# Optimization experiments

Measured on AMD Instinct MI355X. Metric: run time of the kernel, lower is better.

Reference implementation:

```python
import jax, jax.numpy as jnp
import numpy as np

DIM = 1024
HEADS = 16
SEQ = 1024
N_EXP = 2
SLOTS = SEQ // N_EXP  # slots per expert; total slots == seq_len as in SoftMoE(dim, seq_len, num_experts)
HID = 4 * DIM         # expert FFN hidden
EPS = 1e-5


def layernorm(x, g, b):
    mu = x.mean(-1, keepdims=True)
    var = x.var(-1, keepdims=True)
    return (x - mu) * jax.lax.rsqrt(var + EPS) * g + b


def setup_inputs() -> dict:
    key = jax.random.key(0)
    ks = jax.random.split(key, 16)
    s = lambda k, shape, scale=0.02: jax.random.normal(k, shape, jnp.float32) * scale
    return {
        "x": jax.random.normal(ks[0], (4, SEQ, DIM), jnp.float32),
        "Wq": s(ks[1], (DIM, DIM)), "bq": jnp.zeros((DIM,), jnp.float32),
        "Wkv": s(ks[2], (DIM, 2 * DIM)), "bkv": jnp.zeros((2 * DIM,), jnp.float32),
        "Wp": s(ks[3], (DIM, DIM)), "bp": jnp.zeros((DIM,), jnp.float32),
        "g1": jnp.ones((DIM,), jnp.float32), "b1": jnp.zeros((DIM,), jnp.float32),
        "phi": s(ks[4], (DIM, N_EXP, SLOTS)),
        "We1": s(ks[5], (N_EXP, DIM, HID)), "be1": jnp.zeros((N_EXP, HID), jnp.float32),
        "We2": s(ks[6], (N_EXP, HID, DIM)), "be2": jnp.zeros((N_EXP, DIM), jnp.float32),
        "g2": jnp.ones((DIM,), jnp.float32), "b2": jnp.zeros((DIM,), jnp.float32),
    }


def soft_moe(x, phi, We1, be1, We2, be2):
    # x: [b,n,d]; phi: [d,e,s]
    logits = jnp.einsum("bnd,des->bnes", x, phi)
    dispatch = jax.nn.softmax(logits, axis=1)                    # over sequence
    b, n, e, s = logits.shape
    combine = jax.nn.softmax(logits.reshape(b, n, e * s), axis=-1).reshape(b, n, e, s)
    slots = jnp.einsum("bnd,bnes->besd", x, dispatch)            # [b,e,s,d]
    h = jax.nn.gelu(jnp.einsum("besd,edh->besh", slots, We1) + be1[None, :, None, :])
    y = jnp.einsum("besh,ehd->besd", h, We2) + be2[None, :, None, :]
    return jnp.einsum("besd,bnes->bnd", y, combine)


def reference(x, Wq, bq, Wkv, bkv, Wp, bp, g1, b1, phi, We1, be1, We2, be2, g2, b2):
    b, n, c = x.shape
    hd = c // HEADS
    scale = hd ** -0.5
    q = (x @ Wq + bq).reshape(b, n, HEADS, hd)
    kv = (x @ Wkv + bkv).reshape(b, n, 2, HEADS, hd)
    k, v = kv[:, :, 0], kv[:, :, 1]
    attn = jnp.einsum("bnhd,bmhd->bnmh", q, k) * scale
    attn = jax.nn.softmax(attn, axis=2)
    out = jnp.einsum("bnmh,bmhd->bnhd", attn, v).reshape(b, n, c)
    out = out @ Wp + bp
    x1 = layernorm(out + x, g1, b1)
    x2 = x1 + soft_moe(x1, phi, We1, be1, We2, be2)
    y = layernorm(x2 + x1, g2, b2)
    return (y, attn)
```

## Files before the change

### kernel.cpp

```cpp
#include <hip/hip_runtime.h>
#include <math.h>

#define BATCH 4
#define SEQ   1024
#define DIM   1024
#define HEADS 16
#define HD    64
#define NEXP  2
#define NSLOT 512
#define ES    1024
#define HID   4096
#define LNEPS 1e-5f
#define NTOK  (BATCH*SEQ)

typedef long long ll;
typedef unsigned short ushort;
typedef unsigned int uint;
typedef __attribute__((ext_vector_type(8))) short short8;
typedef __attribute__((ext_vector_type(4))) float f32x4;
typedef __attribute__((ext_vector_type(4))) unsigned short us4;

__device__ __forceinline__ ushort f2b(float f) {
    uint u = __builtin_bit_cast(uint, f);
    u += 0x7FFFu + ((u >> 16) & 1u);
    return (ushort)(u >> 16);
}
__device__ __forceinline__ float b2f(ushort h) {
    uint u = ((uint)h) << 16;
    return __builtin_bit_cast(float, u);
}
__device__ __forceinline__ uint pk(float a, float b) {
    return (uint)f2b(a) | ((uint)f2b(b) << 16);
}
__device__ __forceinline__ float gelu_f(float v) {
    float x3 = v * v * v;
    return 0.5f * v * (1.f + tanhf(0.7978845608028654f * (v + 0.044715f * x3)));
}

__device__ __forceinline__ void gload16(const ushort* g, ushort* l) {
    __builtin_amdgcn_global_load_lds(
        (const __attribute__((address_space(1))) unsigned int*)(const void*)g,
        (__attribute__((address_space(3))) unsigned int*)(void*)l,
        16, 0, 0);
}

__global__ __launch_bounds__(256) void cvt_bf16(
    const float* __restrict__ src, ushort* __restrict__ dst)
{
    int i = blockIdx.x * 256 + threadIdx.x;
    const float4* s = reinterpret_cast<const float4*>(src) + (ll)i * 2;
    float4 a = s[0], b = s[1];
    uint4 w;
    w.x = pk(a.x, a.y); w.y = pk(a.z, a.w);
    w.z = pk(b.x, b.y); w.w = pk(b.z, b.w);
    reinterpret_cast<uint4*>(dst)[i] = w;
}

__global__ __launch_bounds__(256) void concat_bias(
    const float* __restrict__ a, const float* __restrict__ b,
    float* __restrict__ o)
{
    int i = blockIdx.x * 256 + threadIdx.x;
    o[i] = (i < DIM) ? a[i] : b[i - DIM];
}

template<typename TS>
__global__ __launch_bounds__(256) void transpose_cvt(
    const TS* __restrict__ src, int ldsrc, ll sS1, ll sS2,
    ushort* __restrict__ dst, int lddst, ll sD1, ll sD2, int Z2)
{
    __shared__ ushort tile[64][68];
    const int z1 = blockIdx.z / Z2, z2 = blockIdx.z % Z2;
    src += z1 * sS1 + z2 * sS2;
    dst += z1 * sD1 + z2 * sD2;
    const int r0 = blockIdx.y * 64, c0 = blockIdx.x * 64;
    const int t = threadIdx.x;
    #pragma unroll
    for (int j = 0; j < 4; j++) {
        int idx = t + 256 * j;
        int r = idx >> 4, c = (idx & 15) * 4;
        if constexpr (sizeof(TS) == 4) {
            float4 v = *reinterpret_cast<const float4*>(src + (ll)(r0 + r) * ldsrc + c0 + c);
            tile[r][c]     = f2b(v.x);
            tile[r][c + 1] = f2b(v.y);
            tile[r][c + 2] = f2b(v.z);
            tile[r][c + 3] = f2b(v.w);
        } else {
            *reinterpret_cast<us4*>(&tile[r][c]) =
                *reinterpret_cast<const us4*>(src + (ll)(r0 + r) * ldsrc + c0 + c);
        }
    }
    __syncthreads();
    #pragma unroll
    for (int j = 0; j < 4; j++) {
        int idx = t + 256 * j;
        int rr = idx >> 4, cc = (idx & 15) * 4;
        us4 w;
        w.x = tile[cc][rr]; w.y = tile[cc + 1][rr];
        w.z = tile[cc + 2][rr]; w.w = tile[cc + 3][rr];
        *reinterpret_cast<us4*>(&dst[(ll)(c0 + rr) * lddst + r0 + cc]) = w;
    }
}

template<int WR, int WC, int MI, int NI, int ACT, typename TC>
__global__ __launch_bounds__(256) void gemm_bf16(
    const ushort* __restrict__ A, int lda, ll sA1, ll sA2,
    const ushort* __restrict__ B, int ldb, ll sB1, ll sB2,
    const float* __restrict__ bias, ll sb1, ll sb2,
    TC* __restrict__ C, int ldc, ll sC1, ll sC2,
    int K, int Z2, float alpha)
{
    constexpr int BM = WR * MI * 16;
    constexpr int BN = WC * NI * 16;
    __shared__ alignas(16) ushort As[BM * 32];
    __shared__ alignas(16) ushort Bs[BN * 32];

    const int z1 = blockIdx.z / Z2, z2 = blockIdx.z % Z2;
    A += z1 * sA1 + z2 * sA2;
    B += z1 * sB1 + z2 * sB2;
    C += z1 * sC1 + z2 * sC2;

    const int t = threadIdx.x;
    const int m0 = blockIdx.y * BM, n0 = blockIdx.x * BN;
    const int lane = t & 63, wave = t >> 6;
    const int quad = lane >> 4, l16 = lane & 15;
    const int wm = wave / WC, wn = wave % WC;

    f32x4 acc[MI][NI] = {};

    for (int k0 = 0; k0 < K; k0 += 32) {
        #pragma unroll
        for (int i = 0; i < BM / 64; i++) {
            int seg = i * 256 + t;
            int row = seg >> 2, ke = (seg & 3) * 8;
            gload16(A + (ll)(m0 + row) * lda + (k0 + ke), &As[seg * 8]);
        }
        #pragma unroll
        for (int i = 0; i < BN / 64; i++) {
            int seg = i * 256 + t;
            int row = seg >> 2, ke = (seg & 3) * 8;
            gload16(B + (ll)(n0 + row) * ldb + (k0 + ke), &Bs[seg * 8]);
        }
        __syncthreads();

        short8 a[MI], b[NI];
        #pragma unroll
        for (int mi = 0; mi < MI; mi++)
            a[mi] = *reinterpret_cast<const short8*>(
                &As[(wm * MI * 16 + mi * 16 + l16) * 32 + quad * 8]);
        #pragma unroll
        for (int ni = 0; ni < NI; ni++)
            b[ni] = *reinterpret_cast<const short8*>(
                &Bs[(wn * NI * 16 + ni * 16 + l16) * 32 + quad * 8]);
        #pragma unroll
        for (int mi = 0; mi < MI; mi++)
            #pragma unroll
            for (int ni = 0; ni < NI; ni++)
                acc[mi][ni] = __builtin_amdgcn_mfma_f32_16x16x32_bf16(
                    a[mi], b[ni], acc[mi][ni], 0, 0, 0);
        __syncthreads();
    }

    const float* bz = bias ? (bias + z1 * sb1 + z2 * sb2) : nullptr;
    #pragma unroll
    for (int mi = 0; mi < MI; mi++) {
        #pragma unroll
        for (int ni = 0; ni < NI; ni++) {
            const int row = m0 + wm * MI * 16 + mi * 16 + quad * 4;
            const int col = n0 + wn * NI * 16 + ni * 16 + l16;
            const float bv = bz ? bz[col] : 0.f;
            #pragma unroll
            for (int r = 0; r < 4; r++) {
                float v = alpha * acc[mi][ni][r] + bv;
                if (ACT) v = gelu_f(v);
                if constexpr (sizeof(TC) == 2)
                    C[(ll)(row + r) * ldc + col] = f2b(v);
                else
                    C[(ll)(row + r) * ldc + col] = v;
            }
        }
    }
}

template<int BM, int BN, int ACT, typename TC>
__global__ __launch_bounds__(512) void gemm2(
    const ushort* __restrict__ A, int lda, ll sA1, ll sA2,
    const ushort* __restrict__ B, int ldb, ll sB1, ll sB2,
    const float* __restrict__ bias, ll sb1, ll sb2,
    TC* __restrict__ C, int ldc, ll sC1, ll sC2,
    int K, int Z2, float alpha)
{
    constexpr int WR = BM / 64;
    constexpr int WC = 8 / WR;
    constexpr int MI = 4;
    constexpr int NI = BN / WC / 16;
    constexpr int NH = NI / 2 ? NI / 2 : 1;
    constexpr int LA = BM / 64;
    constexpr int LB = BN / 64;

    __shared__ alignas(16) ushort As[3][BM * 64];
    __shared__ alignas(16) ushort Bs[3][BN * 64];

    const int z1 = blockIdx.z / Z2, z2 = blockIdx.z % Z2;
    A += z1 * sA1 + z2 * sA2;
    B += z1 * sB1 + z2 * sB2;
    C += z1 * sC1 + z2 * sC2;

    const int t = threadIdx.x;
    const int lane = t & 63, wave = t >> 6;
    const int quad = lane >> 4, l16 = lane & 15;
    const int wm = wave / WC, wn = wave % WC;
    const int m0 = blockIdx.y * BM, n0 = blockIdx.x * BN;

    auto stageA = [&](int kt) {
        const ushort* src = A + (ll)m0 * lda + kt * 64;
        ushort* dst = As[kt % 3];
        #pragma unroll
        for (int j = 0; j < LA; j++) {
            int seg = j * 512 + t;
            int row = seg >> 3, kk = (seg & 7) * 8;
            gload16(src + (ll)row * lda + kk, dst + seg * 8);
        }
    };
    auto stageB = [&](int kt) {
        const ushort* src = B + (ll)n0 * ldb + kt * 64;
        ushort* dst = Bs[kt % 3];
        #pragma unroll
        for (int j = 0; j < LB; j++) {
            int seg = j * 512 + t;
            int row = seg >> 3, kk = (seg & 7) * 8;
            gload16(src + (ll)row * ldb + kk, dst + seg * 8);
        }
    };

    f32x4 acc[MI][NI] = {};
    const int NK = K / 64;

    stageA(0); stageB(0);
    if (NK > 1) { stageA(1); stageB(1); }

    for (int kt = 0; kt < NK; kt++) {
        if (kt + 1 < NK)
            asm volatile("s_waitcnt vmcnt(%0)" :: "n"(LA + LB) : "memory");
        else
            asm volatile("s_waitcnt vmcnt(0)" ::: "memory");
        __builtin_amdgcn_sched_barrier(0);
        __builtin_amdgcn_s_barrier();
        __builtin_amdgcn_sched_barrier(0);

        const ushort* Abuf = As[kt % 3];
        const ushort* Bbuf = Bs[kt % 3];

        short8 a[MI][2], b0[NH][2];
        #pragma unroll
        for (int mi = 0; mi < MI; mi++)
            #pragma unroll
            for (int kh = 0; kh < 2; kh++)
                a[mi][kh] = *reinterpret_cast<const short8*>(
                    &Abuf[(wm * 64 + mi * 16 + l16) * 64 + kh * 32 + quad * 8]);
        #pragma unroll
        for (int ni = 0; ni < NH; ni++)
            #pragma unroll
            for (int kh = 0; kh < 2; kh++)
                b0[ni][kh] = *reinterpret_cast<const short8*>(
                    &Bbuf[(wn * NI * 16 + ni * 16 + l16) * 64 + kh * 32 + quad * 8]);
        if (kt + 2 < NK) stageA(kt + 2);
        asm volatile("s_waitcnt lgkmcnt(0)" ::: "memory");
        __builtin_amdgcn_sched_barrier(0);
        __builtin_amdgcn_s_setprio(1);
        #pragma unroll
        for (int mi = 0; mi < MI; mi++)
            #pragma unroll
            for (int ni = 0; ni < NH; ni++)
                #pragma unroll
                for (int kh = 0; kh < 2; kh++)
                    acc[mi][ni] = __builtin_amdgcn_mfma_f32_16x16x32_bf16(
                        a[mi][kh], b0[ni][kh], acc[mi][ni], 0, 0, 0);
        __builtin_amdgcn_s_setprio(0);
        __builtin_amdgcn_sched_barrier(0);

        short8 b1[NH][2];
        #pragma unroll
        for (int ni = 0; ni < NH; ni++)
            #pragma unroll
            for (int kh = 0; kh < 2; kh++)
                b1[ni][kh] = *reinterpret_cast<const short8*>(
                    &Bbuf[(wn * NI * 16 + (NH + ni) * 16 + l16) * 64 + kh * 32 + quad * 8]);
        if (kt + 2 < NK) stageB(kt + 2);
        asm volatile("s_waitcnt lgkmcnt(0)" ::: "memory");
        __builtin_amdgcn_sched_barrier(0);
        __builtin_amdgcn_s_setprio(1);
        #pragma unroll
        for (int mi = 0; mi < MI; mi++)
            #pragma unroll
            for (int ni = 0; ni < NH; ni++)
                #pragma unroll
                for (int kh = 0; kh < 2; kh++)
                    acc[mi][NH + ni] = __builtin_amdgcn_mfma_f32_16x16x32_bf16(
                        a[mi][kh], b1[ni][kh], acc[mi][NH + ni], 0, 0, 0);
        __builtin_amdgcn_s_setprio(0);
        __builtin_amdgcn_sched_barrier(0);
    }

    const float* bz = bias ? (bias + z1 * sb1 + z2 * sb2) : nullptr;
    #pragma unroll
    for (int mi = 0; mi < MI; mi++) {
        #pragma unroll
        for (int ni = 0; ni < NI; ni++) {
            const int row = m0 + wm * 64 + mi * 16 + quad * 4;
            const int col = n0 + wn * NI * 16 + ni * 16 + l16;
            const float bv = bz ? bz[col] : 0.f;
            #pragma unroll
            for (int r = 0; r < 4; r++) {
                float v = alpha * acc[mi][ni][r] + bv;
                if (ACT) v = gelu_f(v);
                if constexpr (sizeof(TC) == 2)
                    C[(ll)(row + r) * ldc + col] = f2b(v);
                else
                    C[(ll)(row + r) * ldc + col] = v;
            }
        }
    }
}

__global__ __launch_bounds__(256) void attn_softmax(
    ushort* __restrict__ p, float* __restrict__ attn_out)
{
    __shared__ float tile[16][1024];
    const int n = blockIdx.x, b = blockIdx.y;
    const int t = threadIdx.x;
    const int lane = t & 63, w = t >> 6;
    ushort* base = p + ((ll)(b * SEQ + n) * HEADS) * SEQ;
    #pragma unroll 1
    for (int g = 0; g < 4; g++) {
        const int h = g * 4 + w;
        ushort* row = base + (ll)h * SEQ + lane * 16;
        uint4 r0 = reinterpret_cast<const uint4*>(row)[0];
        uint4 r1 = reinterpret_cast<const uint4*>(row)[1];
        uint rr[8] = {r0.x, r0.y, r0.z, r0.w, r1.x, r1.y, r1.z, r1.w};
        float v[16];
        float m = -3.0e38f;
        #pragma unroll
        for (int j = 0; j < 8; j++) {
            v[2 * j]     = b2f((ushort)(rr[j] & 0xFFFFu));
            v[2 * j + 1] = b2f((ushort)(rr[j] >> 16));
            m = fmaxf(m, fmaxf(v[2 * j], v[2 * j + 1]));
        }
        #pragma unroll
        for (int o = 32; o; o >>= 1) m = fmaxf(m, __shfl_xor(m, o));
        float s = 0.f;
        #pragma unroll
        for (int j = 0; j < 16; j++) { v[j] = __expf(v[j] - m); s += v[j]; }
        #pragma unroll
        for (int o = 32; o; o >>= 1) s += __shfl_xor(s, o);
        const float inv = 1.f / s;
        #pragma unroll
        for (int j = 0; j < 16; j++) v[j] *= inv;
        uint pw[8];
        #pragma unroll
        for (int j = 0; j < 8; j++) pw[j] = pk(v[2 * j], v[2 * j + 1]);
        uint4 w0, w1;
        w0.x = pw[0]; w0.y = pw[1]; w0.z = pw[2]; w0.w = pw[3];
        w1.x = pw[4]; w1.y = pw[5]; w1.z = pw[6]; w1.w = pw[7];
        reinterpret_cast<uint4*>(row)[0] = w0;
        reinterpret_cast<uint4*>(row)[1] = w1;
        #pragma unroll
        for (int jj = 0; jj < 4; jj++) {
            float4 f4;
            f4.x = v[4 * jj]; f4.y = v[4 * jj + 1];
            f4.z = v[4 * jj + 2]; f4.w = v[4 * jj + 3];
            *reinterpret_cast<float4*>(&tile[h][(jj * 64 + lane) * 4]) = f4;
        }
    }
    __syncthreads();
    float* outp = attn_out + ((ll)b * SEQ + n) * SEQ * HEADS;
    #pragma unroll
    for (int jj = 0; jj < 4; jj++) {
        const int mm = t + 256 * jj;
        const int gm = mm >> 2;
        const int fi = ((gm & 3) * 64 + (gm >> 2)) * 4 + (mm & 3);
        float o16[16];
        #pragma unroll
        for (int h = 0; h < 16; h++) o16[h] = tile[h][fi];
        float4* dst = reinterpret_cast<float4*>(outp + (ll)mm * HEADS);
        #pragma unroll
        for (int q = 0; q < 4; q++) {
            float4 o4;
            o4.x = o16[4 * q]; o4.y = o16[4 * q + 1];
            o4.z = o16[4 * q + 2]; o4.w = o16[4 * q + 3];
            dst[q] = o4;
        }
    }
}

__global__ __launch_bounds__(256) void ln_kernel(
    const float* __restrict__ a, const float* __restrict__ b, float coef,
    const float* __restrict__ g, const float* __restrict__ beta,
    float* __restrict__ out, ushort* __restrict__ out_bf)
{
    const int row = blockIdx.x;
    const int t = threadIdx.x;
    float4 av = reinterpret_cast<const float4*>(a + (ll)row * DIM)[t];
    float4 bv = reinterpret_cast<const float4*>(b + (ll)row * DIM)[t];
    float4 v;
    v.x = av.x + coef * bv.x; v.y = av.y + coef * bv.y;
    v.z = av.z + coef * bv.z; v.w = av.w + coef * bv.w;
    float s1 = v.x + v.y + v.z + v.w;
    float s2 = v.x * v.x + v.y * v.y + v.z * v.z + v.w * v.w;
    __shared__ float red[8];
    #pragma unroll
    for (int o = 32; o; o >>= 1) { s1 += __shfl_xor(s1, o); s2 += __shfl_xor(s2, o); }
    int w = t >> 6;
    if ((t & 63) == 0) { red[w] = s1; red[4 + w] = s2; }
    __syncthreads();
    s1 = red[0] + red[1] + red[2] + red[3];
    s2 = red[4] + red[5] + red[6] + red[7];
    float mu = s1 * (1.f / DIM);
    float var = s2 * (1.f / DIM) - mu * mu;
    float rs = rsqrtf(var + LNEPS);
    float4 gv = reinterpret_cast<const float4*>(g)[t];
    float4 be = reinterpret_cast<const float4*>(beta)[t];
    float4 o;
    o.x = (v.x - mu) * rs * gv.x + be.x;
    o.y = (v.y - mu) * rs * gv.y + be.y;
    o.z = (v.z - mu) * rs * gv.z + be.z;
    o.w = (v.w - mu) * rs * gv.w + be.w;
    reinterpret_cast<float4*>(out + (ll)row * DIM)[t] = o;
    if (out_bf) {
        us4 hv;
        hv.x = f2b(o.x); hv.y = f2b(o.y); hv.z = f2b(o.z); hv.w = f2b(o.w);
        reinterpret_cast<us4*>(out_bf + (ll)row * DIM)[t] = hv;
    }
}

__global__ __launch_bounds__(256) void col_softmax(
    const float* __restrict__ logits, ushort* __restrict__ dispT)
{
    const int b = blockIdx.x, cc = blockIdx.y;
    const int cl = threadIdx.x & 63;
    const int c = cc * 64 + cl;
    const int rg = threadIdx.x >> 6;
    const float* L = logits + (ll)b * SEQ * ES + c;
    ushort* DT = dispT + (ll)b * ES * SEQ + (ll)c * SEQ;
    __shared__ float red[4][64];
    float m = -3.0e38f;
    for (int n = rg; n < SEQ; n += 4) m = fmaxf(m, L[(ll)n * ES]);
    red[rg][cl] = m;
    __syncthreads();
    m = fmaxf(fmaxf(red[0][cl], red[1][cl]), fmaxf(red[2][cl], red[3][cl]));
    __syncthreads();
    float s = 0.f;
    for (int n = rg; n < SEQ; n += 4) s += __expf(L[(ll)n * ES] - m);
    red[rg][cl] = s;
    __syncthreads();
    s = red[0][cl] + red[1][cl] + red[2][cl] + red[3][cl];
    float inv = 1.f / s;
    for (int n = rg; n < SEQ; n += 4)
        DT[n] = f2b(__expf(L[(ll)n * ES] - m) * inv);
}

__global__ __launch_bounds__(256) void row_softmax(
    const float* __restrict__ logits, ushort* __restrict__ comb)
{
    const int row = blockIdx.x;
    const float* L = logits + (ll)row * ES;
    ushort* O = comb + (ll)row * ES;
    float v[4];
    float m = -3.0e38f;
    #pragma unroll
    for (int j = 0; j < 4; j++) { v[j] = L[threadIdx.x + 256 * j]; m = fmaxf(m, v[j]); }
    __shared__ float red[8];
    #pragma unroll
    for (int o = 32; o; o >>= 1) m = fmaxf(m, __shfl_xor(m, o));
    int w = threadIdx.x >> 6;
    if ((threadIdx.x & 63) == 0) red[w] = m;
    __syncthreads();
    m = fmaxf(fmaxf(red[0], red[1]), fmaxf(red[2], red[3]));
    __syncthreads();
    float s = 0.f;
    #pragma unroll
    for (int j = 0; j < 4; j++) { v[j] = __expf(v[j] - m); s += v[j]; }
    #pragma unroll
    for (int o = 32; o; o >>= 1) s += __shfl_xor(s, o);
    if ((threadIdx.x & 63) == 0) red[4 + w] = s;
    __syncthreads();
    s = red[4] + red[5] + red[6] + red[7];
    float inv = 1.f / s;
    #pragma unroll
    for (int j = 0; j < 4; j++) O[threadIdx.x + 256 * j] = f2b(v[j] * inv);
}

extern "C" void kernel_launch(void* const* d_in, const int* in_sizes, int n_in,
                              void* d_out, int out_size, void* d_ws, size_t ws_size,
                              hipStream_t stream)
{
    const float* x   = (const float*)d_in[0];
    const float* Wq  = (const float*)d_in[1];
    const float* bq  = (const float*)d_in[2];
    const float* Wkv = (const float*)d_in[3];
    const float* bkv = (const float*)d_in[4];
    const float* Wp  = (const float*)d_in[5];
    const float* bp  = (const float*)d_in[6];
    const float* g1  = (const float*)d_in[7];
    const float* b1  = (const float*)d_in[8];
    const float* phi = (const float*)d_in[9];
    const float* We1 = (const float*)d_in[10];
    const float* be1 = (const float*)d_in[11];
    const float* We2 = (const float*)d_in[12];
    const float* be2 = (const float*)d_in[13];
    const float* g2  = (const float*)d_in[14];
    const float* b2  = (const float*)d_in[15];

    float* out_y    = (float*)d_out;
    float* out_attn = out_y + (ll)BATCH * SEQ * DIM;

    const ll M1 = 1024 * 1024;
    float*  ws     = (float*)d_ws;
    ushort* x_bf   = (ushort*)(ws);
    ushort* WqkvT  = (ushort*)(ws + 2 * M1);
    ushort* WpT    = (ushort*)(ws + 7 * M1 / 2);
    ushort* phiT   = (ushort*)(ws + 4 * M1);
    ushort* qkv_bf = (ushort*)(ws + 9 * M1 / 2);
    ushort* vT     = (ushort*)(ws + 21 * M1 / 2);
    ushort* p_bf   = (ushort*)(ws + 25 * M1 / 2);
    float*  po     = ws + 25 * M1 / 2;
    ushort* ao_bf  = (ushort*)(ws + 89 * M1 / 2);
    ushort* ymoeT  = (ushort*)(ws + 89 * M1 / 2);
    float*  x1     = ws + 33 * M1 / 2;
    ushort* x1_bf  = (ushort*)(ws + 41 * M1 / 2);
    ushort* x1T    = (ushort*)(ws + 45 * M1 / 2);
    float*  logit  = ws + 49 * M1 / 2;
    ushort* dispT  = (ushort*)(ws + 57 * M1 / 2);
    ushort* comb   = (ushort*)(ws + 61 * M1 / 2);
    ushort* slots  = (ushort*)(ws + 65 * M1 / 2);
    ushort* hmid   = (ushort*)(ws + 69 * M1 / 2);
    ushort* ymoe   = (ushort*)(ws + 85 * M1 / 2);
    ushort* We1T   = (ushort*)(ws + 9 * M1 / 2);
    ushort* We2T   = (ushort*)(ws + 17 * M1 / 2);
    float*  bqkv   = ws + 93 * M1 / 2;
    float*  moe    = ws;

    dim3 blk(256), blk5(512);

    cvt_bf16<<<dim3(2048), blk, 0, stream>>>(x, x_bf);
    transpose_cvt<float><<<dim3(16, 16, 1), blk, 0, stream>>>(
        Wq, DIM, 0, 0, WqkvT, DIM, 0, 0, 1);
    transpose_cvt<float><<<dim3(32, 16, 1), blk, 0, stream>>>(
        Wkv, 2 * DIM, 0, 0, WqkvT + (ll)DIM * DIM, DIM, 0, 0, 1);
    transpose_cvt<float><<<dim3(16, 16, 1), blk, 0, stream>>>(
        Wp, DIM, 0, 0, WpT, DIM, 0, 0, 1);
    transpose_cvt<float><<<dim3(16, 16, 1), blk, 0, stream>>>(
        phi, ES, 0, 0, phiT, DIM, 0, 0, 1);
    concat_bias<<<dim3(12), blk, 0, stream>>>(bq, bkv, bqkv);

    gemm2<256,128,0,ushort><<<dim3(24, 16, 1), blk5, 0, stream>>>(
        x_bf, DIM, 0, 0, WqkvT, DIM, 0, 0, bqkv, 0, 0,
        qkv_bf, 3 * DIM, 0, 0, DIM, 1, 1.f);

    transpose_cvt<ushort><<<dim3(1, 16, BATCH * HEADS), blk, 0, stream>>>(
        qkv_bf + 2 * DIM, 3 * DIM, (ll)SEQ * 3 * DIM, HD,
        vT, SEQ, (ll)HEADS * HD * SEQ, (ll)HD * SEQ, HEADS);

    gemm_bf16<2,2,4,4,0,ushort><<<dim3(8, 8, BATCH * HEADS), blk, 0, stream>>>(
        qkv_bf, 3 * DIM, (ll)SEQ * 3 * DIM, HD,
        qkv_bf + DIM, 3 * DIM, (ll)SEQ * 3 * DIM, HD,
        nullptr, 0, 0,
        p_bf, HEADS * SEQ, (ll)SEQ * HEADS * SEQ, (ll)SEQ,
        HD, HEADS, 0.125f);

    attn_softmax<<<dim3(SEQ, BATCH), blk, 0, stream>>>(p_bf, out_attn);

    gemm_bf16<4,1,2,4,0,ushort><<<dim3(1, 8, BATCH * HEADS), blk, 0, stream>>>(
        p_bf, HEADS * SEQ, (ll)SEQ * HEADS * SEQ, (ll)SEQ,
        vT, SEQ, (ll)HEADS * HD * SEQ, (ll)HD * SEQ,
        nullptr, 0, 0,
        ao_bf, DIM, (ll)SEQ * DIM, HD,
        SEQ, HEADS, 1.f);

    gemm2<128,128,0,float><<<dim3(8, 32, 1), blk5, 0, stream>>>(
        ao_bf, DIM, 0, 0, WpT, DIM, 0, 0, bp, 0, 0,
        po, DIM, 0, 0, DIM, 1, 1.f);
    ln_kernel<<<dim3(NTOK), blk, 0, stream>>>(po, x, 1.0f, g1, b1, x1, x1_bf);

    transpose_cvt<float><<<dim3(64, 16, 2), blk, 0, stream>>>(
        We1, HID, 0, (ll)DIM * HID, We1T, DIM, 0, (ll)HID * DIM, 2);
    transpose_cvt<float><<<dim3(16, 64, 2), blk, 0, stream>>>(
        We2, DIM, 0, (ll)HID * DIM, We2T, HID, 0, (ll)DIM * HID, 2);
    transpose_cvt<ushort><<<dim3(16, 16, BATCH), blk, 0, stream>>>(
        x1_bf, DIM, (ll)SEQ * DIM, 0, x1T, SEQ, (ll)DIM * SEQ, 0, 1);

    gemm2<128,128,0,float><<<dim3(8, 32, 1), blk5, 0, stream>>>(
        x1_bf, DIM, 0, 0, phiT, DIM, 0, 0, nullptr, 0, 0,
        logit, ES, 0, 0, DIM, 1, 1.f);
    col_softmax<<<dim3(BATCH, 16), blk, 0, stream>>>(logit, dispT);
    row_softmax<<<dim3(NTOK), blk, 0, stream>>>(logit, comb);

    gemm2<128,128,0,ushort><<<dim3(8, 8, BATCH), blk5, 0, stream>>>(
        dispT, SEQ, (ll)ES * SEQ, 0,
        x1T, SEQ, (ll)DIM * SEQ, 0,
        nullptr, 0, 0,
        slots, DIM, (ll)ES * DIM, 0,
        SEQ, 1, 1.f);

    gemm2<256,128,1,ushort><<<dim3(32, 2, BATCH * NEXP), blk5, 0, stream>>>(
        slots, DIM, (ll)ES * DIM, (ll)NSLOT * DIM,
        We1T, DIM, 0, (ll)HID * DIM,
        be1, 0, HID,
        hmid, HID, (ll)ES * HID, (ll)NSLOT * HID,
        DIM, NEXP, 1.f);

    gemm2<128,128,0,ushort><<<dim3(8, 4, BATCH * NEXP), blk5, 0, stream>>>(
        hmid, HID, (ll)ES * HID, (ll)NSLOT * HID,
        We2T, HID, 0, (ll)DIM * HID,
        be2, 0, DIM,
        ymoe, DIM, (ll)ES * DIM, (ll)NSLOT * DIM,
        HID, NEXP, 1.f);

    transpose_cvt<ushort><<<dim3(16, 16, BATCH), blk, 0, stream>>>(
        ymoe, DIM, (ll)ES * DIM, 0, ymoeT, ES, (ll)DIM * ES, 0, 1);

    gemm2<128,128,0,float><<<dim3(8, 8, BATCH), blk5, 0, stream>>>(
        comb, ES, (ll)SEQ * ES, 0,
        ymoeT, ES, (ll)DIM * ES, 0,
        nullptr, 0, 0,
        moe, DIM, (ll)SEQ * DIM, 0,
        ES, 1, 1.f);

    ln_kernel<<<dim3(NTOK), blk, 0, stream>>>(moe, x1, 2.0f, g2, b2, out_y, nullptr);
}
```

Baseline: 1.003 ms.

## Replace column softmax with fp32 transpose plus row softmax; use gemm2 for PV

The column-wise dispatch softmax ran in only 64 blocks with strided loads. It is replaced by an fp32 tiled transpose of the logits into a reused workspace region, followed by the vectorised row softmax kernel over BATCH*ES rows. The transpose kernel is generalised to support a float destination, and row_softmax now uses float4 loads and us4 stores. The attention P·V GEMM also moves from gemm_bf16 to the larger-tile gemm2 kernel. This costs an extra transpose pass over the logits and relies on the po/p_bf workspace region being free at that point.

```diff
diff --git a/kernel.cpp b/kernel.cpp
--- a/kernel.cpp
+++ b/kernel.cpp
@@ -64,12 +64,12 @@
     o[i] = (i < DIM) ? a[i] : b[i - DIM];
 }
 
-template<typename TS>
+template<typename TS, typename TD>
 __global__ __launch_bounds__(256) void transpose_cvt(
     const TS* __restrict__ src, int ldsrc, ll sS1, ll sS2,
-    ushort* __restrict__ dst, int lddst, ll sD1, ll sD2, int Z2)
-{
-    __shared__ ushort tile[64][68];
+    TD* __restrict__ dst, int lddst, ll sD1, ll sD2, int Z2)
+{
+    __shared__ TD tile[64][68];
     const int z1 = blockIdx.z / Z2, z2 = blockIdx.z % Z2;
     src += z1 * sS1 + z2 * sS2;
     dst += z1 * sD1 + z2 * sD2;
@@ -79,12 +79,15 @@
     for (int j = 0; j < 4; j++) {
         int idx = t + 256 * j;
         int r = idx >> 4, c = (idx & 15) * 4;
-        if constexpr (sizeof(TS) == 4) {
+        if constexpr (sizeof(TS) == 4 && sizeof(TD) == 2) {
             float4 v = *reinterpret_cast<const float4*>(src + (ll)(r0 + r) * ldsrc + c0 + c);
             tile[r][c]     = f2b(v.x);
             tile[r][c + 1] = f2b(v.y);
             tile[r][c + 2] = f2b(v.z);
             tile[r][c + 3] = f2b(v.w);
+        } else if constexpr (sizeof(TS) == 4 && sizeof(TD) == 4) {
+            float4 v = *reinterpret_cast<const float4*>(src + (ll)(r0 + r) * ldsrc + c0 + c);
+            *reinterpret_cast<float4*>(&tile[r][c]) = v;
         } else {
             *reinterpret_cast<us4*>(&tile[r][c]) =
                 *reinterpret_cast<const us4*>(src + (ll)(r0 + r) * ldsrc + c0 + c);
@@ -95,10 +98,17 @@
     for (int j = 0; j < 4; j++) {
         int idx = t + 256 * j;
         int rr = idx >> 4, cc = (idx & 15) * 4;
-        us4 w;
-        w.x = tile[cc][rr]; w.y = tile[cc + 1][rr];
-        w.z = tile[cc + 2][rr]; w.w = tile[cc + 3][rr];
-        *reinterpret_cast<us4*>(&dst[(ll)(c0 + rr) * lddst + r0 + cc]) = w;
+        if constexpr (sizeof(TD) == 2) {
+            us4 w;
+            w.x = tile[cc][rr]; w.y = tile[cc + 1][rr];
+            w.z = tile[cc + 2][rr]; w.w = tile[cc + 3][rr];
+            *reinterpret_cast<us4*>(&dst[(ll)(c0 + rr) * lddst + r0 + cc]) = w;
+        } else {
+            float4 w;
+            w.x = tile[cc][rr]; w.y = tile[cc + 1][rr];
+            w.z = tile[cc + 2][rr]; w.w = tile[cc + 3][rr];
+            *reinterpret_cast<float4*>(&dst[(ll)(c0 + rr) * lddst + r0 + cc]) = w;
+        }
     }
 }
 
@@ -433,61 +443,35 @@
     }
 }
 
-__global__ __launch_bounds__(256) void col_softmax(
-    const float* __restrict__ logits, ushort* __restrict__ dispT)
-{
-    const int b = blockIdx.x, cc = blockIdx.y;
-    const int cl = threadIdx.x & 63;
-    const int c = cc * 64 + cl;
-    const int rg = threadIdx.x >> 6;
-    const float* L = logits + (ll)b * SEQ * ES + c;
-    ushort* DT = dispT + (ll)b * ES * SEQ + (ll)c * SEQ;
-    __shared__ float red[4][64];
-    float m = -3.0e38f;
-    for (int n = rg; n < SEQ; n += 4) m = fmaxf(m, L[(ll)n * ES]);
-    red[rg][cl] = m;
-    __syncthreads();
-    m = fmaxf(fmaxf(red[0][cl], red[1][cl]), fmaxf(red[2][cl], red[3][cl]));
-    __syncthreads();
-    float s = 0.f;
-    for (int n = rg; n < SEQ; n += 4) s += __expf(L[(ll)n * ES] - m);
-    red[rg][cl] = s;
-    __syncthreads();
-    s = red[0][cl] + red[1][cl] + red[2][cl] + red[3][cl];
-    float inv = 1.f / s;
-    for (int n = rg; n < SEQ; n += 4)
-        DT[n] = f2b(__expf(L[(ll)n * ES] - m) * inv);
-}
-
 __global__ __launch_bounds__(256) void row_softmax(
     const float* __restrict__ logits, ushort* __restrict__ comb)
 {
     const int row = blockIdx.x;
-    const float* L = logits + (ll)row * ES;
-    ushort* O = comb + (ll)row * ES;
-    float v[4];
-    float m = -3.0e38f;
-    #pragma unroll
-    for (int j = 0; j < 4; j++) { v[j] = L[threadIdx.x + 256 * j]; m = fmaxf(m, v[j]); }
+    const int t = threadIdx.x;
+    float4 v = reinterpret_cast<const float4*>(logits + (ll)row * 1024)[t];
+    float m = fmaxf(fmaxf(v.x, v.y), fmaxf(v.z, v.w));
     __shared__ float red[8];
     #pragma unroll
     for (int o = 32; o; o >>= 1) m = fmaxf(m, __shfl_xor(m, o));
-    int w = threadIdx.x >> 6;
-    if ((threadIdx.x & 63) == 0) red[w] = m;
+    int w = t >> 6;
+    if ((t & 63) == 0) red[w] = m;
     __syncthreads();
     m = fmaxf(fmaxf(red[0], red[1]), fmaxf(red[2], red[3]));
     __syncthreads();
-    float s = 0.f;
-    #pragma unroll
-    for (int j = 0; j < 4; j++) { v[j] = __expf(v[j] - m); s += v[j]; }
+    float4 e;
+    e.x = __expf(v.x - m); e.y = __expf(v.y - m);
+    e.z = __expf(v.z - m); e.w = __expf(v.w - m);
+    float s = e.x + e.y + e.z + e.w;
     #pragma unroll
     for (int o = 32; o; o >>= 1) s += __shfl_xor(s, o);
-    if ((threadIdx.x & 63) == 0) red[4 + w] = s;
+    if ((t & 63) == 0) red[4 + w] = s;
     __syncthreads();
     s = red[4] + red[5] + red[6] + red[7];
     float inv = 1.f / s;
-    #pragma unroll
-    for (int j = 0; j < 4; j++) O[threadIdx.x + 256 * j] = f2b(v[j] * inv);
+    us4 hv;
+    hv.x = f2b(e.x * inv); hv.y = f2b(e.y * inv);
+    hv.z = f2b(e.z * inv); hv.w = f2b(e.w * inv);
+    reinterpret_cast<us4*>(comb + (ll)row * 1024)[t] = hv;
 }
 
 extern "C" void kernel_launch(void* const* d_in, const int* in_sizes, int n_in,
@@ -524,6 +508,7 @@
     ushort* vT     = (ushort*)(ws + 21 * M1 / 2);
     ushort* p_bf   = (ushort*)(ws + 25 * M1 / 2);
     float*  po     = ws + 25 * M1 / 2;
+    float*  logitT = ws + 25 * M1 / 2;
     ushort* ao_bf  = (ushort*)(ws + 89 * M1 / 2);
     ushort* ymoeT  = (ushort*)(ws + 89 * M1 / 2);
     float*  x1     = ws + 33 * M1 / 2;
@@ -543,13 +528,13 @@
     dim3 blk(256), blk5(512);
 
     cvt_bf16<<<dim3(2048), blk, 0, stream>>>(x, x_bf);
-    transpose_cvt<float><<<dim3(16, 16, 1), blk, 0, stream>>>(
+    transpose_cvt<float,ushort><<<dim3(16, 16, 1), blk, 0, stream>>>(
         Wq, DIM, 0, 0, WqkvT, DIM, 0, 0, 1);
-    transpose_cvt<float><<<dim3(32, 16, 1), blk, 0, stream>>>(
+    transpose_cvt<float,ushort><<<dim3(32, 16, 1), blk, 0, stream>>>(
         Wkv, 2 * DIM, 0, 0, WqkvT + (ll)DIM * DIM, DIM, 0, 0, 1);
-    transpose_cvt<float><<<dim3(16, 16, 1), blk, 0, stream>>>(
+    transpose_cvt<float,ushort><<<dim3(16, 16, 1), blk, 0, stream>>>(
         Wp, DIM, 0, 0, WpT, DIM, 0, 0, 1);
-    transpose_cvt<float><<<dim3(16, 16, 1), blk, 0, stream>>>(
+    transpose_cvt<float,ushort><<<dim3(16, 16, 1), blk, 0, stream>>>(
         phi, ES, 0, 0, phiT, DIM, 0, 0, 1);
     concat_bias<<<dim3(12), blk, 0, stream>>>(bq, bkv, bqkv);
 
@@ -557,7 +542,7 @@
         x_bf, DIM, 0, 0, WqkvT, DIM, 0, 0, bqkv, 0, 0,
         qkv_bf, 3 * DIM, 0, 0, DIM, 1, 1.f);
 
-    transpose_cvt<ushort><<<dim3(1, 16, BATCH * HEADS), blk, 0, stream>>>(
+    transpose_cvt<ushort,ushort><<<dim3(1, 16, BATCH * HEADS), blk, 0, stream>>>(
         qkv_bf + 2 * DIM, 3 * DIM, (ll)SEQ * 3 * DIM, HD,
         vT, SEQ, (ll)HEADS * HD * SEQ, (ll)HD * SEQ, HEADS);
 
@@ -570,7 +555,7 @@
 
     attn_softmax<<<dim3(SEQ, BATCH), blk, 0, stream>>>(p_bf, out_attn);
 
-    gemm_bf16<4,1,2,4,0,ushort><<<dim3(1, 8, BATCH * HEADS), blk, 0, stream>>>(
+    gemm2<256,64,0,ushort><<<dim3(1, 4, BATCH * HEADS), blk5, 0, stream>>>(
         p_bf, HEADS * SEQ, (ll)SEQ * HEADS * SEQ, (ll)SEQ,
         vT, SEQ, (ll)HEADS * HD * SEQ, (ll)HD * SEQ,
         nullptr, 0, 0,
@@ -582,17 +567,20 @@
         po, DIM, 0, 0, DIM, 1, 1.f);
     ln_kernel<<<dim3(NTOK), blk, 0, stream>>>(po, x, 1.0f, g1, b1, x1, x1_bf);
 
-    transpose_cvt<float><<<dim3(64, 16, 2), blk, 0, stream>>>(
+    transpose_cvt<float,ushort><<<dim3(64, 16, 2), blk, 0, stream>>>(
         We1, HID, 0, (ll)DIM * HID, We1T, DIM, 0, (ll)HID * DIM, 2);
-    transpose_cvt<float><<<dim3(16, 64, 2), blk, 0, stream>>>(
+    transpose_cvt<float,ushort><<<dim3(16, 64, 2), blk, 0, stream>>>(
         We2, DIM, 0, (ll)HID * DIM, We2T, HID, 0, (ll)DIM * HID, 2);
-    transpose_cvt<ushort><<<dim3(16, 16, BATCH), blk, 0, stream>>>(
+    transpose_cvt<ushort,ushort><<<dim3(16, 16, BATCH), blk, 0, stream>>>(
         x1_bf, DIM, (ll)SEQ * DIM, 0, x1T, SEQ, (ll)DIM * SEQ, 0, 1);
 
     gemm2<128,128,0,float><<<dim3(8, 32, 1), blk5, 0, stream>>>(
         x1_bf, DIM, 0, 0, phiT, DIM, 0, 0, nullptr, 0, 0,
         logit, ES, 0, 0, DIM, 1, 1.f);
-    col_softmax<<<dim3(BATCH, 16), blk, 0, stream>>>(logit, dispT);
+
+    transpose_cvt<float,float><<<dim3(16, 16, BATCH), blk, 0, stream>>>(
+        logit, ES, (ll)SEQ * ES, 0, logitT, SEQ, (ll)ES * SEQ, 0, 1);
+    row_softmax<<<dim3(BATCH * ES), blk, 0, stream>>>(logitT, dispT);
     row_softmax<<<dim3(NTOK), blk, 0, stream>>>(logit, comb);
 
     gemm2<128,128,0,ushort><<<dim3(8, 8, BATCH), blk5, 0, stream>>>(
@@ -616,7 +604,7 @@
         ymoe, DIM, (ll)ES * DIM, (ll)NSLOT * DIM,
         HID, NEXP, 1.f);
 
-    transpose_cvt<ushort><<<dim3(16, 16, BATCH), blk, 0, stream>>>(
+    transpose_cvt<ushort,ushort><<<dim3(16, 16, BATCH), blk, 0, stream>>>(
         ymoe, DIM, (ll)ES * DIM, 0, ymoeT, ES, (ll)DIM * ES, 0, 1);
 
     gemm2<128,128,0,float><<<dim3(8, 8, BATCH), blk5, 0, stream>>>(
```

Result: faster. 883.6 us (-11.9%).
